# Optimization experiments

Measured on AMD Instinct MI355X. Metric: run time of the kernel, lower is better.

Reference implementation:

```python
import jax, jax.numpy as jnp
import numpy as np

B, C, T = 8, 128, 32768
L = 256                 # kernel_length (number of hop segments)
K = 3                   # LVC kernel size
CONV_SIZE = 3           # dilated Conv1d kernel size
DILATION = 3
SLOPE = 0.2             # LeakyReLU slope


def setup_inputs() -> dict:
    key = jax.random.key(0)
    ks = jax.random.split(key, 6)
    x = jax.random.normal(ks[0], (B, C, T), jnp.float32)
    weight = jax.random.normal(ks[1], (B, C, C, K, L), jnp.float32) * 0.05
    bias = jax.random.normal(ks[2], (B, C, L), jnp.float32) * 0.05
    # weight-normalized Conv1d parameters: w = g * v / ||v||_(in,k)
    conv_v = jax.random.normal(ks[3], (C, C, CONV_SIZE), jnp.float32) * 0.05
    conv_g = jnp.ones((C, 1, 1), jnp.float32)
    conv_b = jnp.zeros((C,), jnp.float32)
    return {"x": x, "weight": weight, "bias": bias,
            "conv_v": conv_v, "conv_g": conv_g, "conv_b": conv_b}


def _lvc(x, kernel, bias, hop):
    """Location-variable convolution (dilation=1 path of the torch code).
    x: (B, Cin, T), kernel: (B, Cin, Cout, K, L), bias: (B, Cout, L).
    Returns (B, Cout, T) with T = L * hop.
    """
    pad = (K - 1) // 2
    xp = jnp.pad(x, ((0, 0), (0, 0), (pad, pad)))
    Lk = kernel.shape[-1]
    # segment windows of length hop+2*pad, stride hop  -> (L, hop+2p)
    seg_idx = jnp.arange(Lk)[:, None] * hop + jnp.arange(hop + 2 * pad)[None, :]
    xs = xp[:, :, seg_idx]                                  # (B, Cin, L, hop+2p)
    # sliding windows of length K, stride 1 within each segment -> (hop, K)
    win_idx = jnp.arange(hop)[:, None] + jnp.arange(K)[None, :]
    xw = xs[:, :, :, win_idx]                               # (B, Cin, L, hop, K)
    # per-segment kernel contraction (torch einsum 'bildsk,biokl->bolsd', d==1)
    o = jnp.einsum('bilsk,biokl->bols', xw, kernel)         # (B, Cout, L, hop)
    o = o + bias[:, :, :, None]
    return o.reshape(x.shape[0], kernel.shape[2], -1)       # (B, Cout, T)


def reference(x, weight, bias, conv_v, conv_g, conv_b):
    hop = x.shape[-1] // weight.shape[-1]
    h = _lvc(x, weight, bias, hop)
    h = jax.nn.leaky_relu(h, SLOPE)
    # weight_norm: w = g * v / ||v|| (norm over in_channels and kernel dims)
    vnorm = jnp.sqrt(jnp.sum(conv_v * conv_v, axis=(1, 2), keepdims=True))
    w = conv_g * conv_v / vnorm
    pad = DILATION * (CONV_SIZE - 1) // 2
    h = jax.lax.conv_general_dilated(
        h, w, window_strides=(1,), padding=[(pad, pad)],
        rhs_dilation=(DILATION,), dimension_numbers=('NCH', 'OIH', 'NCH'))
    h = h + conv_b[None, :, None]
    return jax.nn.leaky_relu(h, SLOPE)
```

## Files before the change

kernel.cpp:

```cpp
#include <hip/hip_runtime.h>
#include <hip/hip_bf16.h>

typedef __hip_bfloat16 bf16;

#define BDIM 8
#define CDIM 128
#define TDIM 32768
#define LDIM 256
#define HOP 128
#define SLOPE 0.2f

__device__ __forceinline__ float b2f(bf16 v) { return __bfloat162float(v); }
__device__ __forceinline__ bf16 f2b(float v) { return __float2bfloat16(v); }
__device__ __forceinline__ float lrelu(float v) { return v > 0.f ? v : SLOPE * v; }

__global__ void wnorm_kernel(const float* __restrict__ v, const float* __restrict__ g,
                             float* __restrict__ wn) {
    int c = blockIdx.x;
    int t = threadIdx.x;
    __shared__ float red[128];
    float s = 0.f;
    for (int e = t; e < 384; e += 128) {
        float x = v[c * 384 + e];
        s += x * x;
    }
    red[t] = s;
    __syncthreads();
    for (int off = 64; off > 0; off >>= 1) {
        if (t < off) red[t] += red[t + off];
        __syncthreads();
    }
    float scale = g[c] / sqrtf(red[0]);
    for (int e = t; e < 384; e += 128) {
        wn[c * 384 + e] = scale * v[c * 384 + e];
    }
}

__global__ void __launch_bounds__(256, 2)
lvc_kernel(const float* __restrict__ x, const float* __restrict__ w,
           const float* __restrict__ bias, bf16* __restrict__ h) {
    __shared__ float xseg[CDIM * 130];
    __shared__ float wlds[8 * 3 * CDIM];

    int p = blockIdx.x;
    int b = p >> 8;
    int l = (p & 7) * 32 + ((p >> 3) & 31);
    int t = threadIdx.x;

    int xbase = l * HOP - 1;
    for (int e = t; e < CDIM * 130; e += 256) {
        int i = e / 130;
        int pp = e - i * 130;
        int gpos = xbase + pp;
        float val = 0.f;
        if ((unsigned)gpos < (unsigned)TDIM)
            val = x[(size_t)(b * CDIM + i) * TDIM + gpos];
        xseg[e] = val;
    }

    int sg = t & 31, og = t >> 5;
    int s0 = sg * 4;
    int ob = og * 16;

    float acc[4][16];
#pragma unroll
    for (int u = 0; u < 4; u++)
#pragma unroll
        for (int j = 0; j < 16; j++) acc[u][j] = 0.f;

    for (int ic = 0; ic < 16; ic++) {
        __syncthreads();
        int i0 = ic * 8;
        for (int e = t; e < 3072; e += 256) {
            int ii = e / 384;
            int r = e - ii * 384;
            int o = r / 3;
            int kk = r - o * 3;
            size_t widx = ((((size_t)(b * CDIM + i0 + ii)) * CDIM + o) * 3 + kk) * LDIM + l;
            wlds[(ii * 3 + kk) * CDIM + o] = w[widx];
        }
        __syncthreads();
#pragma unroll
        for (int ii = 0; ii < 8; ii++) {
            int i = i0 + ii;
            const float* xp = &xseg[i * 130 + s0];
            float2 xv01 = *(const float2*)&xp[0];
            float2 xv23 = *(const float2*)&xp[2];
            float2 xv45 = *(const float2*)&xp[4];
            float xv[6] = {xv01.x, xv01.y, xv23.x, xv23.y, xv45.x, xv45.y};
            const float* wp = &wlds[ii * 3 * CDIM + ob];
#pragma unroll
            for (int o4 = 0; o4 < 4; o4++) {
                float4 w0 = *(const float4*)&wp[0 * CDIM + o4 * 4];
                float4 w1 = *(const float4*)&wp[1 * CDIM + o4 * 4];
                float4 w2 = *(const float4*)&wp[2 * CDIM + o4 * 4];
#pragma unroll
                for (int u = 0; u < 4; u++) {
                    float xa = xv[u], xb = xv[u + 1], xc = xv[u + 2];
                    acc[u][o4 * 4 + 0] += w0.x * xa + w1.x * xb + w2.x * xc;
                    acc[u][o4 * 4 + 1] += w0.y * xa + w1.y * xb + w2.y * xc;
                    acc[u][o4 * 4 + 2] += w0.z * xa + w1.z * xb + w2.z * xc;
                    acc[u][o4 * 4 + 3] += w0.w * xa + w1.w * xb + w2.w * xc;
                }
            }
        }
    }

#pragma unroll
    for (int j = 0; j < 16; j++) {
        int o = ob + j;
        float bs = bias[((size_t)b * CDIM + o) * LDIM + l];
        union { ushort4 u4; bf16 v[4]; } pk;
#pragma unroll
        for (int u = 0; u < 4; u++) pk.v[u] = f2b(lrelu(acc[u][j] + bs));
        *(ushort4*)&h[((size_t)(b * CDIM + o)) * TDIM + l * HOP + s0] = pk.u4;
    }
}

__global__ void __launch_bounds__(256, 2)
dconv_kernel(const bf16* __restrict__ hws, const float* __restrict__ wn,
             const float* __restrict__ cb, float* __restrict__ out) {
    __shared__ float ht[CDIM * 134];
    __shared__ float wlds[4 * 3 * CDIM];

    int bid = blockIdx.x;
    int b = bid >> 8;
    int t0 = (bid & 255) * 128;
    int t = threadIdx.x;

    for (int e = t; e < CDIM * 134; e += 256) {
        int i = e / 134;
        int pp = e - i * 134;
        int gpos = t0 + pp - 3;
        float val = 0.f;
        if ((unsigned)gpos < (unsigned)TDIM)
            val = b2f(hws[(size_t)(b * CDIM + i) * TDIM + gpos]);
        ht[e] = val;
    }

    int sg = t & 31, cg = t >> 5;
    int s0 = sg * 4;
    int c0 = cg * 16;

    float acc[4][16];
#pragma unroll
    for (int u = 0; u < 4; u++)
#pragma unroll
        for (int j = 0; j < 16; j++) acc[u][j] = 0.f;

    for (int ic = 0; ic < 32; ic++) {
        __syncthreads();
        int i0 = ic * 4;
        for (int e = t; e < 4 * 3 * CDIM; e += 256) {
            int c = e / 12;
            int r = e - c * 12;
            int ii = r / 3;
            int kk = r - ii * 3;
            wlds[(ii * 3 + kk) * CDIM + c] = wn[c * 384 + (i0 + ii) * 3 + kk];
        }
        __syncthreads();
#pragma unroll
        for (int ii = 0; ii < 4; ii++) {
            int i = i0 + ii;
            const float* hp = &ht[i * 134 + s0];
            float xv[10];
#pragma unroll
            for (int q = 0; q < 5; q++) {
                float2 v2 = *(const float2*)&hp[q * 2];
                xv[q * 2] = v2.x;
                xv[q * 2 + 1] = v2.y;
            }
            const float* wp = &wlds[ii * 3 * CDIM + c0];
#pragma unroll
            for (int o4 = 0; o4 < 4; o4++) {
                float4 w0 = *(const float4*)&wp[0 * CDIM + o4 * 4];
                float4 w1 = *(const float4*)&wp[1 * CDIM + o4 * 4];
                float4 w2 = *(const float4*)&wp[2 * CDIM + o4 * 4];
#pragma unroll
                for (int u = 0; u < 4; u++) {
                    float xa = xv[u], xb = xv[u + 3], xc = xv[u + 6];
                    acc[u][o4 * 4 + 0] += w0.x * xa + w1.x * xb + w2.x * xc;
                    acc[u][o4 * 4 + 1] += w0.y * xa + w1.y * xb + w2.y * xc;
                    acc[u][o4 * 4 + 2] += w0.z * xa + w1.z * xb + w2.z * xc;
                    acc[u][o4 * 4 + 3] += w0.w * xa + w1.w * xb + w2.w * xc;
                }
            }
        }
    }

#pragma unroll
    for (int j = 0; j < 16; j++) {
        int c = c0 + j;
        float bc = cb[c];
        float4 pk;
        pk.x = lrelu(acc[0][j] + bc);
        pk.y = lrelu(acc[1][j] + bc);
        pk.z = lrelu(acc[2][j] + bc);
        pk.w = lrelu(acc[3][j] + bc);
        *(float4*)&out[((size_t)(b * CDIM + c)) * TDIM + t0 + s0] = pk;
    }
}

extern "C" void kernel_launch(void* const* d_in, const int* in_sizes, int n_in,
                              void* d_out, int out_size, void* d_ws, size_t ws_size,
                              hipStream_t stream) {
    const float* x      = (const float*)d_in[0];
    const float* weight = (const float*)d_in[1];
    const float* bias   = (const float*)d_in[2];
    const float* conv_v = (const float*)d_in[3];
    const float* conv_g = (const float*)d_in[4];
    const float* conv_b = (const float*)d_in[5];
    float* out = (float*)d_out;

    float* wn = (float*)d_ws;
    bf16* h = (bf16*)((char*)d_ws + (size_t)262144);

    wnorm_kernel<<<dim3(128), dim3(128), 0, stream>>>(conv_v, conv_g, wn);
    lvc_kernel<<<dim3(2048), dim3(256), 0, stream>>>(x, weight, bias, h);
    dconv_kernel<<<dim3(2048), dim3(256), 0, stream>>>(h, wn, conv_b, out);
}
```

Before: 2.881 ms.

## Restructure LVC tiling for coalesced weight loads and double-buffer weights in both convs

The LVC kernel is retiled so each block covers 16 segments by 4 output channels. It reads contiguous runs of 16 segments from the weight tensor with vectorized nontemporal loads, replacing the strided per-element gather. x is now read straight from global memory instead of being staged in LDS. Both kernels double-buffer the weight tile in LDS with register prefetch, the dilated conv keeps h as bf16 in LDS and decodes it with bit shifts, and the weight-norm output is pre-transposed for contiguous loads. In exchange, x is reloaded once per output-channel group, and the occupancy bounds and grid size change.

```diff
diff --git a/kernel.cpp b/kernel.cpp
--- a/kernel.cpp
+++ b/kernel.cpp
@@ -2,20 +2,17 @@
 #include <hip/hip_bf16.h>
 
 typedef __hip_bfloat16 bf16;
-
-#define BDIM 8
-#define CDIM 128
-#define TDIM 32768
-#define LDIM 256
-#define HOP 128
+typedef float f4 __attribute__((ext_vector_type(4)));
+
 #define SLOPE 0.2f
 
-__device__ __forceinline__ float b2f(bf16 v) { return __bfloat162float(v); }
+__device__ __forceinline__ float lrelu(float v) { return v > 0.f ? v : SLOPE * v; }
 __device__ __forceinline__ bf16 f2b(float v) { return __float2bfloat16(v); }
-__device__ __forceinline__ float lrelu(float v) { return v > 0.f ? v : SLOPE * v; }
+__device__ __forceinline__ float blo(unsigned u) { return __uint_as_float(u << 16); }
+__device__ __forceinline__ float bhi(unsigned u) { return __uint_as_float(u & 0xffff0000u); }
 
 __global__ void wnorm_kernel(const float* __restrict__ v, const float* __restrict__ g,
-                             float* __restrict__ wn) {
+                             float* __restrict__ wnt) {
     int c = blockIdx.x;
     int t = threadIdx.x;
     __shared__ float red[128];
@@ -32,71 +29,181 @@
     }
     float scale = g[c] / sqrtf(red[0]);
     for (int e = t; e < 384; e += 128) {
-        wn[c * 384 + e] = scale * v[c * 384 + e];
-    }
-}
-
-__global__ void __launch_bounds__(256, 2)
+        wnt[e * 128 + c] = scale * v[c * 384 + e];
+    }
+}
+
+#define ICH 8
+
+__global__ void __launch_bounds__(256, 4)
 lvc_kernel(const float* __restrict__ x, const float* __restrict__ w,
            const float* __restrict__ bias, bf16* __restrict__ h) {
-    __shared__ float xseg[CDIM * 130];
-    __shared__ float wlds[8 * 3 * CDIM];
-
-    int p = blockIdx.x;
-    int b = p >> 8;
-    int l = (p & 7) * 32 + ((p >> 3) & 31);
-    int t = threadIdx.x;
-
-    int xbase = l * HOP - 1;
-    for (int e = t; e < CDIM * 130; e += 256) {
-        int i = e / 130;
-        int pp = e - i * 130;
-        int gpos = xbase + pp;
-        float val = 0.f;
-        if ((unsigned)gpos < (unsigned)TDIM)
-            val = x[(size_t)(b * CDIM + i) * TDIM + gpos];
-        xseg[e] = val;
-    }
-
-    int sg = t & 31, og = t >> 5;
-    int s0 = sg * 4;
-    int ob = og * 16;
+    __shared__ float wls[2][ICH * 4 * 3 * 16];
+
+    int p   = blockIdx.x;
+    int xcd = p & 7, j = p >> 3;
+    int g   = xcd * 16 + (j >> 5);
+    int oq  = j & 31;
+    int b = g >> 4, lg = g & 15;
+    int tid = threadIdx.x;
+    int l_loc = tid & 15, sq = tid >> 4;
+    int s0 = sq * 8;
+    int o0 = oq * 4;
+    int tbase = lg * 2048;
+    int l = lg * 16 + l_loc;
+
+    const float* xbase_t = x + (size_t)b * 128 * 32768 + (tbase + l_loc * 128 + s0 - 1);
+    bool guardL = (lg == 0) && (tid == 0);
+    bool guardR = (lg == 15) && (tid == 255);
+
+    f4 wpre0, wpre1;
+
+#define LVC_LOADW(icn) do {                                                          \
+        { int e4 = tid; int ll4 = e4 & 3; int r = e4 >> 2;                           \
+          int kk = r % 3; int oo = (r / 3) & 3; int ii2 = r / 12;                    \
+          wpre0 = __builtin_nontemporal_load((const f4*)&w[                          \
+              ((((size_t)(b * 128 + (icn) * ICH + ii2)) * 128 + o0 + oo) * 3 + kk) * 256 \
+              + lg * 16 + ll4 * 4]); }                                               \
+        if (tid < 128) {                                                             \
+          int e4 = tid + 256; int ll4 = e4 & 3; int r = e4 >> 2;                     \
+          int kk = r % 3; int oo = (r / 3) & 3; int ii2 = r / 12;                    \
+          wpre1 = __builtin_nontemporal_load((const f4*)&w[                          \
+              ((((size_t)(b * 128 + (icn) * ICH + ii2)) * 128 + o0 + oo) * 3 + kk) * 256 \
+              + lg * 16 + ll4 * 4]); }                                               \
+    } while (0)
+
+#define LVC_WRITEW(nb) do {                                                          \
+        *(f4*)&wls[nb][tid * 4] = wpre0;                                             \
+        if (tid < 128) *(f4*)&wls[nb][(tid + 256) * 4] = wpre1;                      \
+    } while (0)
+
+    float acc[4][8];
+#pragma unroll
+    for (int o = 0; o < 4; o++)
+#pragma unroll
+        for (int u = 0; u < 8; u++) acc[o][u] = 0.f;
+
+    LVC_LOADW(0);
+    LVC_WRITEW(0);
+    __syncthreads();
+
+    for (int ic = 0; ic < 16; ic++) {
+        int cur = ic & 1;
+        if (ic < 15) LVC_LOADW(ic + 1);
+        const float* wp = wls[cur];
+#pragma unroll
+        for (int ii = 0; ii < ICH; ii++) {
+            const float* xrow = xbase_t + (size_t)(ic * ICH + ii) * 32768;
+            float xw0 = 0.f, xw9 = 0.f;
+            if (!guardL) xw0 = xrow[0];
+            if (!guardR) xw9 = xrow[9];
+            f4 xa = *(const f4*)(xrow + 1);
+            f4 xb = *(const f4*)(xrow + 5);
+            float xw[10] = {xw0, xa.x, xa.y, xa.z, xa.w, xb.x, xb.y, xb.z, xb.w, xw9};
+#pragma unroll
+            for (int o = 0; o < 4; o++) {
+                float w0 = wp[((ii * 4 + o) * 3 + 0) * 16 + l_loc];
+                float w1 = wp[((ii * 4 + o) * 3 + 1) * 16 + l_loc];
+                float w2 = wp[((ii * 4 + o) * 3 + 2) * 16 + l_loc];
+#pragma unroll
+                for (int u = 0; u < 8; u++)
+                    acc[o][u] += w0 * xw[u] + w1 * xw[u + 1] + w2 * xw[u + 2];
+            }
+        }
+        if (ic < 15) LVC_WRITEW(cur ^ 1);
+        __syncthreads();
+    }
+
+#pragma unroll
+    for (int o = 0; o < 4; o++) {
+        float bs = bias[((size_t)(b * 128 + o0 + o)) * 256 + l];
+        union { bf16 bv[8]; ushort4 v4[2]; } pk;
+#pragma unroll
+        for (int u = 0; u < 8; u++) pk.bv[u] = f2b(lrelu(acc[o][u] + bs));
+        bf16* hp = h + ((size_t)(b * 128 + o0 + o)) * 32768 + tbase + l_loc * 128 + s0;
+        *(ushort4*)&hp[0] = pk.v4[0];
+        *(ushort4*)&hp[4] = pk.v4[1];
+    }
+}
+
+#define DICH 4
+
+__global__ void __launch_bounds__(256, 3)
+dconv_kernel(const bf16* __restrict__ hws, const float* __restrict__ wnt,
+             const float* __restrict__ cb, float* __restrict__ out) {
+    __shared__ ushort ht[128][136];
+    __shared__ float wls[2][DICH * 3 * 128];
+
+    int bid = blockIdx.x;
+    int b = bid >> 8;
+    int tb = (bid & 255) * 128;
+    int tid = threadIdx.x;
+    int sg = tid & 31, cg = tid >> 5;
+    int s0 = sg * 4, c0 = cg * 16;
+
+    const ushort* hbase = (const ushort*)hws + (size_t)b * 128 * 32768;
+#pragma unroll
+    for (int q = 0; q < 16; q++) {
+        int e = tid + 256 * q;
+        int i = e >> 5, m = e & 31;
+        ushort4 val = *(const ushort4*)&hbase[(size_t)i * 32768 + tb + 4 * m];
+        *(ushort4*)&ht[i][4 + 4 * m] = val;
+    }
+    if (tid < 128) {
+        const ushort* hrow = hbase + (size_t)tid * 32768;
+#pragma unroll
+        for (int d = 0; d < 3; d++) {
+            int gl = tb - 3 + d;
+            ht[tid][1 + d] = (gl >= 0) ? hrow[gl] : (ushort)0;
+            int gr = tb + 128 + d;
+            ht[tid][132 + d] = (gr < 32768) ? hrow[gr] : (ushort)0;
+        }
+    }
+
+    f4 wq0, wq1;
+#define DC_LOADW(icn) do {                                                   \
+        wq0 = *(const f4*)&wnt[(icn) * 1536 + tid * 4];                      \
+        if (tid < 128) wq1 = *(const f4*)&wnt[(icn) * 1536 + (tid + 256) * 4]; \
+    } while (0)
+#define DC_WRITEW(nb) do {                                                   \
+        *(f4*)&wls[nb][tid * 4] = wq0;                                       \
+        if (tid < 128) *(f4*)&wls[nb][(tid + 256) * 4] = wq1;                \
+    } while (0)
+
+    DC_LOADW(0);
+    DC_WRITEW(0);
 
     float acc[4][16];
 #pragma unroll
     for (int u = 0; u < 4; u++)
 #pragma unroll
-        for (int j = 0; j < 16; j++) acc[u][j] = 0.f;
-
-    for (int ic = 0; ic < 16; ic++) {
-        __syncthreads();
-        int i0 = ic * 8;
-        for (int e = t; e < 3072; e += 256) {
-            int ii = e / 384;
-            int r = e - ii * 384;
-            int o = r / 3;
-            int kk = r - o * 3;
-            size_t widx = ((((size_t)(b * CDIM + i0 + ii)) * CDIM + o) * 3 + kk) * LDIM + l;
-            wlds[(ii * 3 + kk) * CDIM + o] = w[widx];
-        }
-        __syncthreads();
-#pragma unroll
-        for (int ii = 0; ii < 8; ii++) {
-            int i = i0 + ii;
-            const float* xp = &xseg[i * 130 + s0];
-            float2 xv01 = *(const float2*)&xp[0];
-            float2 xv23 = *(const float2*)&xp[2];
-            float2 xv45 = *(const float2*)&xp[4];
-            float xv[6] = {xv01.x, xv01.y, xv23.x, xv23.y, xv45.x, xv45.y};
-            const float* wp = &wlds[ii * 3 * CDIM + ob];
+        for (int n = 0; n < 16; n++) acc[u][n] = 0.f;
+
+    __syncthreads();
+
+    for (int ic = 0; ic < 32; ic++) {
+        int cur = ic & 1;
+        if (ic < 31) DC_LOADW(ic + 1);
+#pragma unroll
+        for (int ii = 0; ii < DICH; ii++) {
+            int i = ic * DICH + ii;
+            uint2 q0 = *(const uint2*)&ht[i][s0];
+            uint2 q1 = *(const uint2*)&ht[i][s0 + 4];
+            uint2 q2 = *(const uint2*)&ht[i][s0 + 8];
+            float xf[11];
+            xf[0] = 0.f;
+            xf[1] = bhi(q0.x); xf[2] = blo(q0.y); xf[3] = bhi(q0.y);
+            xf[4] = blo(q1.x); xf[5] = bhi(q1.x); xf[6] = blo(q1.y); xf[7] = bhi(q1.y);
+            xf[8] = blo(q2.x); xf[9] = bhi(q2.x); xf[10] = blo(q2.y);
+            const float* wp = &wls[cur][ii * 3 * 128 + c0];
 #pragma unroll
             for (int o4 = 0; o4 < 4; o4++) {
-                float4 w0 = *(const float4*)&wp[0 * CDIM + o4 * 4];
-                float4 w1 = *(const float4*)&wp[1 * CDIM + o4 * 4];
-                float4 w2 = *(const float4*)&wp[2 * CDIM + o4 * 4];
+                float4 w0 = *(const float4*)&wp[0 * 128 + o4 * 4];
+                float4 w1 = *(const float4*)&wp[1 * 128 + o4 * 4];
+                float4 w2 = *(const float4*)&wp[2 * 128 + o4 * 4];
 #pragma unroll
                 for (int u = 0; u < 4; u++) {
-                    float xa = xv[u], xb = xv[u + 1], xc = xv[u + 2];
+                    float xa = xf[u + 1], xb = xf[u + 4], xc = xf[u + 7];
                     acc[u][o4 * 4 + 0] += w0.x * xa + w1.x * xb + w2.x * xc;
                     acc[u][o4 * 4 + 1] += w0.y * xa + w1.y * xb + w2.y * xc;
                     acc[u][o4 * 4 + 2] += w0.z * xa + w1.z * xb + w2.z * xc;
@@ -104,100 +211,20 @@
                 }
             }
         }
-    }
-
-#pragma unroll
-    for (int j = 0; j < 16; j++) {
-        int o = ob + j;
-        float bs = bias[((size_t)b * CDIM + o) * LDIM + l];
-        union { ushort4 u4; bf16 v[4]; } pk;
-#pragma unroll
-        for (int u = 0; u < 4; u++) pk.v[u] = f2b(lrelu(acc[u][j] + bs));
-        *(ushort4*)&h[((size_t)(b * CDIM + o)) * TDIM + l * HOP + s0] = pk.u4;
-    }
-}
-
-__global__ void __launch_bounds__(256, 2)
-dconv_kernel(const bf16* __restrict__ hws, const float* __restrict__ wn,
-             const float* __restrict__ cb, float* __restrict__ out) {
-    __shared__ float ht[CDIM * 134];
-    __shared__ float wlds[4 * 3 * CDIM];
-
-    int bid = blockIdx.x;
-    int b = bid >> 8;
-    int t0 = (bid & 255) * 128;
-    int t = threadIdx.x;
-
-    for (int e = t; e < CDIM * 134; e += 256) {
-        int i = e / 134;
-        int pp = e - i * 134;
-        int gpos = t0 + pp - 3;
-        float val = 0.f;
-        if ((unsigned)gpos < (unsigned)TDIM)
-            val = b2f(hws[(size_t)(b * CDIM + i) * TDIM + gpos]);
-        ht[e] = val;
-    }
-
-    int sg = t & 31, cg = t >> 5;
-    int s0 = sg * 4;
-    int c0 = cg * 16;
-
-    float acc[4][16];
-#pragma unroll
-    for (int u = 0; u < 4; u++)
-#pragma unroll
-        for (int j = 0; j < 16; j++) acc[u][j] = 0.f;
-
-    for (int ic = 0; ic < 32; ic++) {
+        if (ic < 31) DC_WRITEW(cur ^ 1);
         __syncthreads();
-        int i0 = ic * 4;
-        for (int e = t; e < 4 * 3 * CDIM; e += 256) {
-            int c = e / 12;
-            int r = e - c * 12;
-            int ii = r / 3;
-            int kk = r - ii * 3;
-            wlds[(ii * 3 + kk) * CDIM + c] = wn[c * 384 + (i0 + ii) * 3 + kk];
-        }
-        __syncthreads();
-#pragma unroll
-        for (int ii = 0; ii < 4; ii++) {
-            int i = i0 + ii;
-            const float* hp = &ht[i * 134 + s0];
-            float xv[10];
-#pragma unroll
-            for (int q = 0; q < 5; q++) {
-                float2 v2 = *(const float2*)&hp[q * 2];
-                xv[q * 2] = v2.x;
-                xv[q * 2 + 1] = v2.y;
-            }
-            const float* wp = &wlds[ii * 3 * CDIM + c0];
-#pragma unroll
-            for (int o4 = 0; o4 < 4; o4++) {
-                float4 w0 = *(const float4*)&wp[0 * CDIM + o4 * 4];
-                float4 w1 = *(const float4*)&wp[1 * CDIM + o4 * 4];
-                float4 w2 = *(const float4*)&wp[2 * CDIM + o4 * 4];
-#pragma unroll
-                for (int u = 0; u < 4; u++) {
-                    float xa = xv[u], xb = xv[u + 3], xc = xv[u + 6];
-                    acc[u][o4 * 4 + 0] += w0.x * xa + w1.x * xb + w2.x * xc;
-                    acc[u][o4 * 4 + 1] += w0.y * xa + w1.y * xb + w2.y * xc;
-                    acc[u][o4 * 4 + 2] += w0.z * xa + w1.z * xb + w2.z * xc;
-                    acc[u][o4 * 4 + 3] += w0.w * xa + w1.w * xb + w2.w * xc;
-                }
-            }
-        }
-    }
-
-#pragma unroll
-    for (int j = 0; j < 16; j++) {
-        int c = c0 + j;
+    }
+
+#pragma unroll
+    for (int n = 0; n < 16; n++) {
+        int c = c0 + n;
         float bc = cb[c];
         float4 pk;
-        pk.x = lrelu(acc[0][j] + bc);
-        pk.y = lrelu(acc[1][j] + bc);
-        pk.z = lrelu(acc[2][j] + bc);
-        pk.w = lrelu(acc[3][j] + bc);
-        *(float4*)&out[((size_t)(b * CDIM + c)) * TDIM + t0 + s0] = pk;
+        pk.x = lrelu(acc[0][n] + bc);
+        pk.y = lrelu(acc[1][n] + bc);
+        pk.z = lrelu(acc[2][n] + bc);
+        pk.w = lrelu(acc[3][n] + bc);
+        *(float4*)&out[((size_t)(b * 128 + c)) * 32768 + tb + s0] = pk;
     }
 }
 
@@ -212,10 +239,10 @@
     const float* conv_b = (const float*)d_in[5];
     float* out = (float*)d_out;
 
-    float* wn = (float*)d_ws;
+    float* wnt = (float*)d_ws;
     bf16* h = (bf16*)((char*)d_ws + (size_t)262144);
 
-    wnorm_kernel<<<dim3(128), dim3(128), 0, stream>>>(conv_v, conv_g, wn);
-    lvc_kernel<<<dim3(2048), dim3(256), 0, stream>>>(x, weight, bias, h);
-    dconv_kernel<<<dim3(2048), dim3(256), 0, stream>>>(h, wn, conv_b, out);
-}
+    wnorm_kernel<<<dim3(128), dim3(128), 0, stream>>>(conv_v, conv_g, wnt);
+    lvc_kernel<<<dim3(4096), dim3(256), 0, stream>>>(x, weight, bias, h);
+    dconv_kernel<<<dim3(2048), dim3(256), 0, stream>>>(h, wnt, conv_b, out);
+}
```

Result: slower. 10.11 ms (+250.8%).
